# Optimization experiments

Hardware: AMD Instinct MI355X
Metric: run time of the kernel (lower is better)

## Reference

```python
import jax, jax.numpy as jnp
from jax import lax
import numpy as np

BN_EPS = 1e-3  # ultralytics BatchNorm2d default eps

def setup_inputs() -> dict:
    key = jax.random.key(0)
    ks = jax.random.split(key, 6)
    B, C, H, W = 16, 64, 160, 160
    E, R = 4, 16  # experts, reduced router dim = C // reduction
    return {
        "x": jax.random.normal(ks[0], (B, C, H, W), jnp.float32),
        "fc1_w": jax.random.normal(ks[1], (R, C), jnp.float32) * 0.1,
        "fc2_w": jax.random.normal(ks[2], (E, R), jnp.float32) * 0.1,
        "fc2_b": jax.random.normal(ks[3], (E,), jnp.float32) * 0.1,
        "conv_w": jax.random.normal(ks[4], (E, C, C, 3, 3), jnp.float32) * 0.05,
        "bn_gamma": jnp.ones((E, C), jnp.float32),
        "bn_beta": jnp.zeros((E, C), jnp.float32),
        "bn_mean": jax.random.normal(ks[5], (E, C), jnp.float32) * 0.1,
        "bn_var": jnp.ones((E, C), jnp.float32),
    }

def reference(x, fc1_w, fc2_w, fc2_b, conv_w, bn_gamma, bn_beta, bn_mean, bn_var):
    # Router: global avg pool -> fc1 -> relu -> fc2 -> softmax over experts
    g = jnp.mean(x, axis=(2, 3))                       # [B, C]
    h = jax.nn.relu(g @ fc1_w.T)                       # [B, R]
    w = jax.nn.softmax(h @ fc2_w.T + fc2_b, axis=1)    # [B, E]

    def expert(kernel, gamma, beta, mean, var):
        # Conv2d(bias=False, pad=k//2) + BatchNorm2d (eval) + SiLU
        y = lax.conv_general_dilated(
            x, kernel, window_strides=(1, 1), padding="SAME",
            dimension_numbers=("NCHW", "OIHW", "NCHW"))
        scale = (gamma * lax.rsqrt(var + BN_EPS))[None, :, None, None]
        shift = (beta - mean * gamma * lax.rsqrt(var + BN_EPS))[None, :, None, None]
        return jax.nn.silu(y * scale + shift)          # [B, Co, H, W]

    outs = jax.vmap(expert)(conv_w, bn_gamma, bn_beta, bn_mean, bn_var)  # [E, B, Co, H, W]
    return jnp.einsum("ebchw,be->bchw", outs, w)
```

## Files before the change

kernel.cpp:

```cpp
#include <hip/hip_runtime.h>
#include <hip/hip_bf16.h>

typedef unsigned short u16;
typedef unsigned int   u32;
typedef __attribute__((ext_vector_type(8))) short s16x8;
typedef __attribute__((ext_vector_type(4))) float f32x4;

#define BN_EPS 1e-3f
#define NB 16
#define NC 64
#define NH 160
#define NW 160
#define NE 4
#define NR 16
#define HP 162
#define WPD 162

#define OFF_XT 0UL
#define SZ_XT  (16UL*162*162*64*2)
#define OFF_WT (OFF_XT + SZ_XT)
#define SZ_WT  (4UL*64*9*64*2)
#define OFF_SC (OFF_WT + SZ_WT)
#define OFF_SH (OFF_SC + 1024UL)
#define OFF_G  (OFF_SH + 1024UL)
#define OFF_WE (OFF_G + 4096UL)
#define OFF_GP (OFF_WE + 256UL)

#define XLS_BYTES (340 * 64 * 2)
#define WLS_BYTES (2304 * 16)
#define SMEM_TOTAL (XLS_BYTES + WLS_BYTES)

__device__ __forceinline__ u16 f2bf(float f) {
    u32 u = __builtin_bit_cast(u32, f);
    u += 0x7fffu + ((u >> 16) & 1u);
    return (u16)(u >> 16);
}

__global__ void zero_border(u16* __restrict__ xt) {
    int blk = blockIdx.x;
    int hp = blk % 162, b = blk / 162;
    u32* row = (u32*)xt + (((long)b * 162 + hp) * 162) * 32;
    int t = threadIdx.x;
    if (hp == 0 || hp == 161) {
        for (int i = t; i < 162 * 32; i += 256) row[i] = 0u;
    } else if (t < 64) {
        int p = (t >> 5) ? 161 : 0;
        row[p * 32 + (t & 31)] = 0u;
    }
}

__global__ void prep_w(const float* __restrict__ cw, u16* __restrict__ wt,
                       const float* __restrict__ gamma, const float* __restrict__ beta,
                       const float* __restrict__ mean, const float* __restrict__ var,
                       float* __restrict__ scale, float* __restrict__ shift) {
    int idx = blockIdx.x * 256 + threadIdx.x;
    if (idx < 4 * 2 * 9 * 4 * 64 * 8) {
        int cin = idx & 7;
        int t = idx >> 3;
        int co = t & 63; t >>= 6;
        int cio = t & 3; t >>= 2;
        int tap = t % 9; t /= 9;
        int ch = t & 1;
        int e = t >> 1;
        int ci = ch * 32 + cio * 8 + cin;
        wt[idx] = f2bf(cw[(((long)(e * 64 + co)) * 64 + ci) * 9 + tap]);
    }
    if (idx < 256) {
        float sc = gamma[idx] * rsqrtf(var[idx] + BN_EPS);
        scale[idx] = sc;
        shift[idx] = beta[idx] - mean[idx] * sc;
    }
}

__global__ void prep_x(const float* __restrict__ x, u16* __restrict__ xt,
                       float* __restrict__ gpart) {
    __shared__ float tile[64][33];
    int blk = blockIdx.x;
    int wt5 = blk % 5;
    int tmp = blk / 5;
    int h = tmp % 160, b = tmp / 160;
    int w0 = wt5 * 32;
    int t = threadIdx.x;
    int w = t & 31, c0 = t >> 5;
#pragma unroll
    for (int i = 0; i < 8; ++i) {
        int c = c0 + 8 * i;
        tile[c][w] = x[(((long)b * 64 + c) * 160 + h) * 160 + w0 + w];
    }
    __syncthreads();
    if (t < 64) {
        float s = 0.f;
#pragma unroll
        for (int wi = 0; wi < 32; ++wi) s += tile[t][wi];
        gpart[((long)(b * 64 + t)) * 800 + h * 5 + wt5] = s;
    }
    u32* xt32 = (u32*)xt;
    long base = ((((long)b * 162 + h + 1) * 162) + (w0 + 1)) * 32;
#pragma unroll
    for (int j = 0; j < 4; ++j) {
        int idx = t + 256 * j;
        int p = idx >> 5, cp = idx & 31;
        float v0 = tile[2 * cp][p], v1 = tile[2 * cp + 1][p];
        xt32[base + p * 32 + cp] = (u32)f2bf(v0) | ((u32)f2bf(v1) << 16);
    }
}

__global__ void g_reduce(const float* __restrict__ gpart, float* __restrict__ g) {
    int id = blockIdx.x;
    int t = threadIdx.x;
    float s = 0.f;
    for (int i = t; i < 800; i += 256) s += gpart[(long)id * 800 + i];
#pragma unroll
    for (int off = 32; off > 0; off >>= 1) s += __shfl_down(s, off, 64);
    __shared__ float red[4];
    if ((t & 63) == 0) red[t >> 6] = s;
    __syncthreads();
    if (t == 0) g[id] = (red[0] + red[1] + red[2] + red[3]) * (1.f / 25600.f);
}

__global__ void router(const float* __restrict__ g, const float* __restrict__ fc1w,
                       const float* __restrict__ fc2w, const float* __restrict__ fc2b,
                       float* __restrict__ wexp) {
    __shared__ float gL[16][64];
    __shared__ float h1[16][16];
    __shared__ float z[16][4];
    int t = threadIdx.x;
    for (int i = t; i < 1024; i += 256) gL[i >> 6][i & 63] = g[i];
    __syncthreads();
    {
        int b = t >> 4, r = t & 15;
        float s = 0.f;
#pragma unroll
        for (int c = 0; c < 64; ++c) s += gL[b][c] * fc1w[r * 64 + c];
        h1[b][r] = fmaxf(s, 0.f);
    }
    __syncthreads();
    if (t < 64) {
        int b = t >> 2, e = t & 3;
        float s = fc2b[e];
#pragma unroll
        for (int r = 0; r < 16; ++r) s += h1[b][r] * fc2w[e * 16 + r];
        z[b][e] = s;
    }
    __syncthreads();
    if (t < 16) {
        int b = t;
        float m = fmaxf(fmaxf(z[b][0], z[b][1]), fmaxf(z[b][2], z[b][3]));
        float e0 = __expf(z[b][0] - m), e1 = __expf(z[b][1] - m);
        float e2 = __expf(z[b][2] - m), e3 = __expf(z[b][3] - m);
        float inv = 1.f / (e0 + e1 + e2 + e3);
        wexp[b * 4 + 0] = e0 * inv; wexp[b * 4 + 1] = e1 * inv;
        wexp[b * 4 + 2] = e2 * inv; wexp[b * 4 + 3] = e3 * inv;
    }
}

__global__ __launch_bounds__(256, 2) void conv_main(
    const u16* __restrict__ xt, const u16* __restrict__ wt,
    const float* __restrict__ scale, const float* __restrict__ shift,
    const float* __restrict__ wexp, float* __restrict__ out) {
    extern __shared__ char smem[];
    u16* xls = (u16*)smem;
    u16* wls = (u16*)(smem + XLS_BYTES);

    const int o = blockIdx.x;
    const int blk = (o & 7) * 200 + (o >> 3);
    const int wt5 = blk % 5;
    const int tmp = blk / 5;
    const int ht = tmp % 20;
    const int b = tmp / 20;
    const int h0 = ht * 8, w0 = wt5 * 32;
    const int tid = threadIdx.x;
    const int lane = tid & 63;
    const int wv = tid >> 6;
    const int l15 = lane & 15, kl = lane >> 4;

    {
        const u16* xb = xt + (long)b * HP * WPD * 64;
        for (int c = tid; c < 2720; c += 256) {
            int P = c >> 3, cg = c & 7;
            int y = P / 34, px = P - y * 34;
            const u16* src = xb + (((long)(h0 + y) * WPD) + (w0 + px)) * 64 + cg * 8;
            s16x8 v = *(const s16x8*)src;
            *(s16x8*)(&xls[(cg * 340 + P) << 3]) = v;
        }
    }

    int Pbase[4];
#pragma unroll
    for (int nf = 0; nf < 4; ++nf)
        Pbase[nf] = (2 * wv + (nf >> 1)) * 34 + (nf & 1) * 16 + l15;

    int oB[2][4];
#pragma unroll
    for (int ch = 0; ch < 2; ++ch)
#pragma unroll
        for (int nf = 0; nf < 4; ++nf)
            oB[ch][nf] = (((ch * 4 + kl) * 340) + Pbase[nf]) << 3;
    const int oA = (kl * 64 + l15) << 3;

    f32x4 oacc[4][4];
#pragma unroll
    for (int i = 0; i < 4; ++i)
#pragma unroll
        for (int j = 0; j < 4; ++j) oacc[i][j] = (f32x4)(0.f);

#pragma unroll 1
    for (int e = 0; e < 4; ++e) {
        f32x4 acc[4][4];
#pragma unroll
        for (int i = 0; i < 4; ++i)
#pragma unroll
            for (int j = 0; j < 4; ++j) acc[i][j] = (f32x4)(0.f);

#pragma unroll 1
        for (int ch = 0; ch < 2; ++ch) {
            __syncthreads();
            {
                const u16* wsrc = wt + ((long)(e * 2 + ch)) * 2304 * 8;
#pragma unroll
                for (int r = 0; r < 9; ++r) {
                    int oo = r * 256 + tid;
                    __builtin_amdgcn_global_load_lds(
                        (const __attribute__((address_space(1))) void*)(wsrc + oo * 8),
                        (__attribute__((address_space(3))) void*)(wls + oo * 8),
                        16, 0, 0);
                }
            }
            __syncthreads();

#pragma unroll
            for (int tap = 0; tap < 9; ++tap) {
                const int dy = tap / 3, dx = tap - 3 * dy;
                const int poff8 = (dy * 34 + dx) << 3;
                const int at = oA + tap * 2048;
                s16x8 af0 = *(const s16x8*)(&wls[at]);
                s16x8 af1 = *(const s16x8*)(&wls[at + 128]);
                s16x8 af2 = *(const s16x8*)(&wls[at + 256]);
                s16x8 af3 = *(const s16x8*)(&wls[at + 384]);
                s16x8 bf0 = *(const s16x8*)(&xls[oB[ch][0] + poff8]);
                s16x8 bf1 = *(const s16x8*)(&xls[oB[ch][1] + poff8]);
                s16x8 bf2 = *(const s16x8*)(&xls[oB[ch][2] + poff8]);
                s16x8 bf3 = *(const s16x8*)(&xls[oB[ch][3] + poff8]);
                acc[0][0] = __builtin_amdgcn_mfma_f32_16x16x32_bf16(af0, bf0, acc[0][0], 0, 0, 0);
                acc[1][0] = __builtin_amdgcn_mfma_f32_16x16x32_bf16(af1, bf0, acc[1][0], 0, 0, 0);
                acc[2][0] = __builtin_amdgcn_mfma_f32_16x16x32_bf16(af2, bf0, acc[2][0], 0, 0, 0);
                acc[3][0] = __builtin_amdgcn_mfma_f32_16x16x32_bf16(af3, bf0, acc[3][0], 0, 0, 0);
                acc[0][1] = __builtin_amdgcn_mfma_f32_16x16x32_bf16(af0, bf1, acc[0][1], 0, 0, 0);
                acc[1][1] = __builtin_amdgcn_mfma_f32_16x16x32_bf16(af1, bf1, acc[1][1], 0, 0, 0);
                acc[2][1] = __builtin_amdgcn_mfma_f32_16x16x32_bf16(af2, bf1, acc[2][1], 0, 0, 0);
                acc[3][1] = __builtin_amdgcn_mfma_f32_16x16x32_bf16(af3, bf1, acc[3][1], 0, 0, 0);
                acc[0][2] = __builtin_amdgcn_mfma_f32_16x16x32_bf16(af0, bf2, acc[0][2], 0, 0, 0);
                acc[1][2] = __builtin_amdgcn_mfma_f32_16x16x32_bf16(af1, bf2, acc[1][2], 0, 0, 0);
                acc[2][2] = __builtin_amdgcn_mfma_f32_16x16x32_bf16(af2, bf2, acc[2][2], 0, 0, 0);
                acc[3][2] = __builtin_amdgcn_mfma_f32_16x16x32_bf16(af3, bf2, acc[3][2], 0, 0, 0);
                acc[0][3] = __builtin_amdgcn_mfma_f32_16x16x32_bf16(af0, bf3, acc[0][3], 0, 0, 0);
                acc[1][3] = __builtin_amdgcn_mfma_f32_16x16x32_bf16(af1, bf3, acc[1][3], 0, 0, 0);
                acc[2][3] = __builtin_amdgcn_mfma_f32_16x16x32_bf16(af2, bf3, acc[2][3], 0, 0, 0);
                acc[3][3] = __builtin_amdgcn_mfma_f32_16x16x32_bf16(af3, bf3, acc[3][3], 0, 0, 0);
            }
        }
        const float we = wexp[(b << 2) + e];
#pragma unroll
        for (int mf = 0; mf < 4; ++mf) {
#pragma unroll
            for (int j = 0; j < 4; ++j) {
                const int co = mf * 16 + (kl << 2) + j;
                const float sc = scale[(e << 6) + co];
                const float sh = shift[(e << 6) + co];
#pragma unroll
                for (int nf = 0; nf < 4; ++nf) {
                    float y = acc[mf][nf][j] * sc + sh;
                    float s = y * __builtin_amdgcn_rcpf(1.f + __expf(-y));
                    oacc[mf][nf][j] += we * s;
                }
            }
        }
    }
#pragma unroll
    for (int mf = 0; mf < 4; ++mf) {
#pragma unroll
        for (int nf = 0; nf < 4; ++nf) {
            const int y = h0 + 2 * wv + (nf >> 1);
            const int x = w0 + (nf & 1) * 16 + l15;
#pragma unroll
            for (int j = 0; j < 4; ++j) {
                const int co = mf * 16 + (kl << 2) + j;
                out[(((long)(b * 64 + co)) * 160 + y) * 160 + x] = oacc[mf][nf][j];
            }
        }
    }
}

extern "C" void kernel_launch(void* const* d_in, const int* in_sizes, int n_in,
                              void* d_out, int out_size, void* d_ws, size_t ws_size,
                              hipStream_t stream) {
    const float* x = (const float*)d_in[0];
    const float* fc1w = (const float*)d_in[1];
    const float* fc2w = (const float*)d_in[2];
    const float* fc2b = (const float*)d_in[3];
    const float* convw = (const float*)d_in[4];
    const float* gamma = (const float*)d_in[5];
    const float* beta = (const float*)d_in[6];
    const float* mean = (const float*)d_in[7];
    const float* var = (const float*)d_in[8];
    float* out = (float*)d_out;
    char* ws = (char*)d_ws;
    u16* xt = (u16*)(ws + OFF_XT);
    u16* wtb = (u16*)(ws + OFF_WT);
    float* scale = (float*)(ws + OFF_SC);
    float* shift = (float*)(ws + OFF_SH);
    float* g = (float*)(ws + OFF_G);
    float* wexp = (float*)(ws + OFF_WE);
    float* gpart = (float*)(ws + OFF_GP);

    hipFuncSetAttribute((const void*)conv_main,
                        hipFuncAttributeMaxDynamicSharedMemorySize, SMEM_TOTAL);

    zero_border<<<16 * 162, 256, 0, stream>>>(xt);
    prep_w<<<576, 256, 0, stream>>>(convw, wtb, gamma, beta, mean, var, scale, shift);
    prep_x<<<12800, 256, 0, stream>>>(x, xt, gpart);
    g_reduce<<<1024, 256, 0, stream>>>(gpart, g);
    router<<<1, 256, 0, stream>>>(g, fc1w, fc2w, fc2b, wexp);
    conv_main<<<1600, 256, SMEM_TOTAL, stream>>>(xt, wtb, scale, shift, wexp, out);
}
```

Before: 183.0 us.

## Split weight-load wait to overlap taps, pad LDS stride, fold border zeroing

Replaces the full barrier after the async weight load with two partial vmcnt waits, so the first five taps start once their weights have arrived while the rest are still loading. The activation LDS channel-group stride is padded from 340 to 342 to change the bank mapping, and the border-zeroing kernel is merged into prep_x as extra blocks to save a launch. The hand-encoded waitcnt values depend on the order of the global_load_lds instructions and on how many loads are still outstanding, so a wrong count could read stale weights.

```diff
diff --git a/kernel.cpp b/kernel.cpp
--- a/kernel.cpp
+++ b/kernel.cpp
@@ -26,7 +26,8 @@
 #define OFF_WE (OFF_G + 4096UL)
 #define OFF_GP (OFF_WE + 256UL)
 
-#define XLS_BYTES (340 * 64 * 2)
+#define XSTRIDE 342
+#define XLS_BYTES (8 * XSTRIDE * 16)
 #define WLS_BYTES (2304 * 16)
 #define SMEM_TOTAL (XLS_BYTES + WLS_BYTES)
 
@@ -34,19 +35,6 @@
     u32 u = __builtin_bit_cast(u32, f);
     u += 0x7fffu + ((u >> 16) & 1u);
     return (u16)(u >> 16);
-}
-
-__global__ void zero_border(u16* __restrict__ xt) {
-    int blk = blockIdx.x;
-    int hp = blk % 162, b = blk / 162;
-    u32* row = (u32*)xt + (((long)b * 162 + hp) * 162) * 32;
-    int t = threadIdx.x;
-    if (hp == 0 || hp == 161) {
-        for (int i = t; i < 162 * 32; i += 256) row[i] = 0u;
-    } else if (t < 64) {
-        int p = (t >> 5) ? 161 : 0;
-        row[p * 32 + (t & 31)] = 0u;
-    }
 }
 
 __global__ void prep_w(const float* __restrict__ cw, u16* __restrict__ wt,
@@ -76,11 +64,23 @@
                        float* __restrict__ gpart) {
     __shared__ float tile[64][33];
     int blk = blockIdx.x;
+    int t = threadIdx.x;
+    if (blk >= 12800) {
+        int bb = blk - 12800;
+        int hp = bb % 162, b = bb / 162;
+        u32* row = (u32*)xt + (((long)b * 162 + hp) * 162) * 32;
+        if (hp == 0 || hp == 161) {
+            for (int i = t; i < 162 * 32; i += 256) row[i] = 0u;
+        } else if (t < 64) {
+            int p = (t >> 5) ? 161 : 0;
+            row[p * 32 + (t & 31)] = 0u;
+        }
+        return;
+    }
     int wt5 = blk % 5;
     int tmp = blk / 5;
     int h = tmp % 160, b = tmp / 160;
     int w0 = wt5 * 32;
-    int t = threadIdx.x;
     int w = t & 31, c0 = t >> 5;
 #pragma unroll
     for (int i = 0; i < 8; ++i) {
@@ -181,7 +181,7 @@
             int y = P / 34, px = P - y * 34;
             const u16* src = xb + (((long)(h0 + y) * WPD) + (w0 + px)) * 64 + cg * 8;
             s16x8 v = *(const s16x8*)src;
-            *(s16x8*)(&xls[(cg * 340 + P) << 3]) = v;
+            *(s16x8*)(&xls[(cg * XSTRIDE + P) << 3]) = v;
         }
     }
 
@@ -190,12 +190,6 @@
     for (int nf = 0; nf < 4; ++nf)
         Pbase[nf] = (2 * wv + (nf >> 1)) * 34 + (nf & 1) * 16 + l15;
 
-    int oB[2][4];
-#pragma unroll
-    for (int ch = 0; ch < 2; ++ch)
-#pragma unroll
-        for (int nf = 0; nf < 4; ++nf)
-            oB[ch][nf] = (((ch * 4 + kl) * 340) + Pbase[nf]) << 3;
     const int oA = (kl * 64 + l15) << 3;
 
     f32x4 oacc[4][4];
@@ -226,10 +220,12 @@
                         16, 0, 0);
                 }
             }
-            __syncthreads();
-
-#pragma unroll
-            for (int tap = 0; tap < 9; ++tap) {
+            int oB0 = (((ch * 4 + kl) * XSTRIDE) + Pbase[0]) << 3;
+            int oB1 = (((ch * 4 + kl) * XSTRIDE) + Pbase[1]) << 3;
+            int oB2 = (((ch * 4 + kl) * XSTRIDE) + Pbase[2]) << 3;
+            int oB3 = (((ch * 4 + kl) * XSTRIDE) + Pbase[3]) << 3;
+
+            auto tap_body = [&](int tap) {
                 const int dy = tap / 3, dx = tap - 3 * dy;
                 const int poff8 = (dy * 34 + dx) << 3;
                 const int at = oA + tap * 2048;
@@ -237,10 +233,10 @@
                 s16x8 af1 = *(const s16x8*)(&wls[at + 128]);
                 s16x8 af2 = *(const s16x8*)(&wls[at + 256]);
                 s16x8 af3 = *(const s16x8*)(&wls[at + 384]);
-                s16x8 bf0 = *(const s16x8*)(&xls[oB[ch][0] + poff8]);
-                s16x8 bf1 = *(const s16x8*)(&xls[oB[ch][1] + poff8]);
-                s16x8 bf2 = *(const s16x8*)(&xls[oB[ch][2] + poff8]);
-                s16x8 bf3 = *(const s16x8*)(&xls[oB[ch][3] + poff8]);
+                s16x8 bf0 = *(const s16x8*)(&xls[oB0 + poff8]);
+                s16x8 bf1 = *(const s16x8*)(&xls[oB1 + poff8]);
+                s16x8 bf2 = *(const s16x8*)(&xls[oB2 + poff8]);
+                s16x8 bf3 = *(const s16x8*)(&xls[oB3 + poff8]);
                 acc[0][0] = __builtin_amdgcn_mfma_f32_16x16x32_bf16(af0, bf0, acc[0][0], 0, 0, 0);
                 acc[1][0] = __builtin_amdgcn_mfma_f32_16x16x32_bf16(af1, bf0, acc[1][0], 0, 0, 0);
                 acc[2][0] = __builtin_amdgcn_mfma_f32_16x16x32_bf16(af2, bf0, acc[2][0], 0, 0, 0);
@@ -257,7 +253,19 @@
                 acc[1][3] = __builtin_amdgcn_mfma_f32_16x16x32_bf16(af1, bf3, acc[1][3], 0, 0, 0);
                 acc[2][3] = __builtin_amdgcn_mfma_f32_16x16x32_bf16(af2, bf3, acc[2][3], 0, 0, 0);
                 acc[3][3] = __builtin_amdgcn_mfma_f32_16x16x32_bf16(af3, bf3, acc[3][3], 0, 0, 0);
-            }
+            };
+
+            __builtin_amdgcn_s_waitcnt(0x074);
+            __builtin_amdgcn_s_barrier();
+            __builtin_amdgcn_sched_barrier(0);
+#pragma unroll
+            for (int tap = 0; tap < 5; ++tap) tap_body(tap);
+
+            __builtin_amdgcn_s_waitcnt(0xF70);
+            __builtin_amdgcn_s_barrier();
+            __builtin_amdgcn_sched_barrier(0);
+#pragma unroll
+            for (int tap = 5; tap < 9; ++tap) tap_body(tap);
         }
         const float we = wexp[(b << 2) + e];
 #pragma unroll
@@ -316,9 +324,8 @@
     hipFuncSetAttribute((const void*)conv_main,
                         hipFuncAttributeMaxDynamicSharedMemorySize, SMEM_TOTAL);
 
-    zero_border<<<16 * 162, 256, 0, stream>>>(xt);
     prep_w<<<576, 256, 0, stream>>>(convw, wtb, gamma, beta, mean, var, scale, shift);
-    prep_x<<<12800, 256, 0, stream>>>(x, xt, gpart);
+    prep_x<<<15392, 256, 0, stream>>>(x, xt, gpart);
     g_reduce<<<1024, 256, 0, stream>>>(gpart, g);
     router<<<1, 256, 0, stream>>>(g, fc1w, fc2w, fc2b, wexp);
     conv_main<<<1600, 256, SMEM_TOTAL, stream>>>(xt, wtb, scale, shift, wexp, out);
```

New measurement: 177.1 us. 3.2% less time.
